# Kernel optimization log

Measured on AMD Instinct MI355X. Metric: run time of the kernel, lower is better.

## Reference

```python
import jax, jax.numpy as jnp
import numpy as np

N = 100_000   # nodes
D = 64        # hidden = H * C
H, C = 8, 8   # heads, per-head channels
E = 500_000   # edges per edge set
EPS = 1e-3    # keras LayerNormalization default epsilon
RSQRT_C = np.float32(1.0 / np.sqrt(C))


def setup_inputs() -> dict:
    key = jax.random.key(0)
    ks = jax.random.split(key, 13)
    s = 0.05
    return dict(
        x=jax.random.normal(ks[0], (N, D), jnp.float32),
        src0=jax.random.randint(ks[1], (E,), 0, N, jnp.int32),
        dst0=jax.random.randint(ks[2], (E,), 0, N, jnp.int32),
        src1=jax.random.randint(ks[3], (E,), 0, N, jnp.int32),
        dst1=jax.random.randint(ks[4], (E,), 0, N, jnp.int32),
        Wk=jax.random.normal(ks[5], (D, D), jnp.float32) * s,
        bk=jnp.zeros((D,), jnp.float32),
        Wm=jax.random.normal(ks[6], (D, D), jnp.float32) * s,
        bm=jnp.zeros((D,), jnp.float32),
        Wq=jax.random.normal(ks[7], (D, D), jnp.float32) * s,
        bq=jnp.zeros((D,), jnp.float32),
        Wa=jax.random.normal(ks[8], (D, D), jnp.float32) * s,
        ba=jnp.zeros((D,), jnp.float32),
        Watt0=jax.random.normal(ks[9], (H, C, C), jnp.float32) * s,
        Wmsg0=jax.random.normal(ks[10], (H, C, C), jnp.float32) * s,
        prior0=jnp.ones((H,), jnp.float32),
        Watt1=jax.random.normal(ks[11], (H, C, C), jnp.float32) * s,
        Wmsg1=jax.random.normal(ks[12], (H, C, C), jnp.float32) * s,
        prior1=jnp.ones((H,), jnp.float32),
        skip_w=jnp.ones((1,), jnp.float32),
        ln_gamma=jnp.ones((D,), jnp.float32),
        ln_beta=jnp.zeros((D,), jnp.float32),
    )


def _edge_terms(k, m, q, src, dst, Watt, Wmsg, prior):
    # gather sender keys/messages, apply per-edge-set per-head projections
    ke = jnp.einsum('ehk,hkl->ehl', k[src], Watt)          # [E,H,C]
    score = jnp.einsum('ehc,ehc->eh', ke, q[dst]) * prior * RSQRT_C  # [E,H]
    me = jnp.einsum('ehk,hkl->ehl', m[src], Wmsg)          # [E,H,C]
    return score, me


def _forward(x, src0, dst0, src1, dst1, Wk, bk, Wm, bm, Wq, bq, Wa, ba,
             Watt0, Wmsg0, prior0, Watt1, Wmsg1, prior1,
             skip_w, ln_gamma, ln_beta):
    n = x.shape[0]
    split = lambda t: t.reshape(n, H, C)
    k = split(x @ Wk + bk)   # sender keys   [N,H,C]
    m = split(x @ Wm + bm)   # sender msgs   [N,H,C]
    q = split(x @ Wq + bq)   # receiver qrys [N,H,C]

    s0, m0 = _edge_terms(k, m, q, src0, dst0, Watt0, Wmsg0, prior0)
    s1, m1 = _edge_terms(k, m, q, src1, dst1, Watt1, Wmsg1, prior1)

    # joint segment softmax over ALL incoming edges per receiver (across edge sets)
    scores = jnp.concatenate([s0, s1], axis=0)  # [Et,H]
    msgs = jnp.concatenate([m0, m1], axis=0)    # [Et,H,C]
    recv = jnp.concatenate([dst0, dst1], axis=0)
    smax = jax.ops.segment_max(scores, recv, num_segments=n)
    ex = jnp.exp(scores - smax[recv])
    denom = jax.ops.segment_sum(ex, recv, num_segments=n)
    coef = ex / denom[recv]                      # [Et,H]

    pooled = jax.ops.segment_sum(coef[:, :, None] * msgs, recv, num_segments=n)  # [N,H,C]
    merged = pooled.reshape(n, D)
    agg = jax.nn.gelu(merged, approximate=False) @ Wa + ba
    # (dropout_rate=0.0 -> identity)
    sc = jax.nn.sigmoid(skip_w[0])               # learnable weighted skip
    out = sc * agg + (1.0 - sc) * x
    # layer norm (keras default eps=1e-3)
    mu = jnp.mean(out, axis=-1, keepdims=True)
    var = jnp.var(out, axis=-1, keepdims=True)
    return ln_gamma * (out - mu) * jax.lax.rsqrt(var + EPS) + ln_beta


def reference(x, src0, dst0, src1, dst1, Wk, bk, Wm, bm, Wq, bq, Wa, ba,
              Watt0, Wmsg0, prior0, Watt1, Wmsg1, prior1,
              skip_w, ln_gamma, ln_beta):
    return _forward(x, src0, dst0, src1, dst1, Wk, bk, Wm, bm, Wq, bq, Wa, ba,
                    Watt0, Wmsg0, prior0, Watt1, Wmsg1, prior1,
                    skip_w, ln_gamma, ln_beta)
```

## Files before the change

kernel.cpp:

```cpp
#include <hip/hip_runtime.h>
#include <cstdint>
#include <cstddef>

#define TPB 256
static constexpr float RSQRT_C_F = 0.35355339059327373f;

typedef __attribute__((ext_vector_type(8))) short bf16x8;
typedef __attribute__((ext_vector_type(4))) float f32x4;

__device__ __forceinline__ unsigned short f2bf(float f) {
    unsigned u = __float_as_uint(f);
    u += 0x7FFFu + ((u >> 16) & 1u);
    return (unsigned short)(u >> 16);
}
__device__ __forceinline__ float bf2f(unsigned short h) {
    return __uint_as_float((unsigned)h << 16);
}
__device__ __forceinline__ float loF(unsigned u) { return __uint_as_float(u << 16); }
__device__ __forceinline__ float hiF(unsigned u) { return __uint_as_float(u); }

__global__ void prep1_kernel(const float* __restrict__ Wq, const float* __restrict__ bq,
                             const float* __restrict__ Wk, const float* __restrict__ bk,
                             const float* __restrict__ Wm, const float* __restrict__ bm,
                             const float* __restrict__ Watt0, const float* __restrict__ prior0,
                             const float* __restrict__ Watt1, const float* __restrict__ prior1,
                             const float* __restrict__ Wmsg0, const float* __restrict__ Wmsg1,
                             float* __restrict__ Wbig, float* __restrict__ bbig) {
    int idx = blockIdx.x * TPB + threadIdx.x;
    if (idx < 64 * 320) {
        int i = idx / 320, col = idx % 320;
        float v;
        if (col < 64) {
            v = Wq[i * 64 + col];
        } else {
            int j = col - 64, set = j >> 6, l = j & 63, h = l >> 3, lc = l & 7;
            const float* Win = (set < 2) ? Wk : Wm;
            const float* T = (set == 0) ? Watt0 : (set == 1) ? Watt1 : (set == 2) ? Wmsg0 : Wmsg1;
            float scale = (set == 0) ? prior0[h] * RSQRT_C_F
                        : (set == 1) ? prior1[h] * RSQRT_C_F : 1.f;
            float acc = 0.f;
            #pragma unroll
            for (int c = 0; c < 8; c++) acc += Win[i * 64 + h * 8 + c] * T[h * 64 + c * 8 + lc];
            v = acc * scale;
        }
        Wbig[idx] = v;
    } else if (idx < 64 * 320 + 320) {
        int col = idx - 64 * 320;
        float v;
        if (col < 64) {
            v = bq[col];
        } else {
            int j = col - 64, set = j >> 6, l = j & 63, h = l >> 3, lc = l & 7;
            const float* bin = (set < 2) ? bk : bm;
            const float* T = (set == 0) ? Watt0 : (set == 1) ? Watt1 : (set == 2) ? Wmsg0 : Wmsg1;
            float scale = (set == 0) ? prior0[h] * RSQRT_C_F
                        : (set == 1) ? prior1[h] * RSQRT_C_F : 1.f;
            float acc = 0.f;
            #pragma unroll
            for (int c = 0; c < 8; c++) acc += bin[h * 8 + c] * T[h * 64 + c * 8 + lc];
            v = acc * scale;
        }
        bbig[col] = v;
    }
}

__global__ void prep2_kernel(const float* __restrict__ Wbig, const float* __restrict__ Wa,
                             unsigned short* __restrict__ Wpack,
                             unsigned short* __restrict__ Wapack) {
    int p = blockIdx.x * TPB + threadIdx.x;
    bool isWa = (p >= 40 * 64);
    if (p >= 48 * 64) return;
    int pl = isWa ? p - 40 * 64 : p;
    int lane = pl & 63, ctkt = pl >> 6;
    int ct = ctkt >> 1, kt = ctkt & 1;
    int kbase = kt * 32 + (lane >> 4) * 8;
    int col = ct * 16 + (lane & 15);
    const float* W = isWa ? Wa : Wbig;
    const int stride = isWa ? 64 : 320;
    unsigned short h[8];
    #pragma unroll
    for (int j = 0; j < 8; j++) h[j] = f2bf(W[(size_t)(kbase + j) * stride + col]);
    uint4 pk;
    pk.x = (unsigned)h[0] | ((unsigned)h[1] << 16);
    pk.y = (unsigned)h[2] | ((unsigned)h[3] << 16);
    pk.z = (unsigned)h[4] | ((unsigned)h[5] << 16);
    pk.w = (unsigned)h[6] | ((unsigned)h[7] << 16);
    unsigned short* dst = isWa ? Wapack : Wpack;
    *(uint4*)&dst[(size_t)pl * 8] = pk;
}

__global__ void hist_kernel(const int* __restrict__ dst0, const int* __restrict__ dst1,
                            int* __restrict__ sub, int* __restrict__ rank,
                            int E0, int Etot, int N) {
    int e = blockIdx.x * TPB + threadIdx.x;
    if (e >= Etot) return;
    int d = (e < E0) ? dst0[e] : dst1[e - E0];
    d = min(max(d, 0), N - 1);
    int s = blockIdx.x & 7;
    rank[e] = atomicAdd(&sub[s * N + d], 1);
}

__global__ void sumsub_kernel(int* __restrict__ sub, int* __restrict__ count, int N) {
    int d = blockIdx.x * TPB + threadIdx.x;
    if (d >= N) return;
    int s = 0;
    #pragma unroll
    for (int b = 0; b < 8; b++) {
        int t = sub[b * N + d];
        sub[b * N + d] = s;
        s += t;
    }
    count[d] = s;
}

__global__ void scan1(const int* __restrict__ count, int* __restrict__ offsets,
                      int* __restrict__ blocksums, int n) {
    __shared__ int sums[TPB];
    int b = blockIdx.x, t = threadIdx.x;
    int base = b * 1024 + t * 4;
    int c0 = (base + 0 < n) ? count[base + 0] : 0;
    int c1 = (base + 1 < n) ? count[base + 1] : 0;
    int c2 = (base + 2 < n) ? count[base + 2] : 0;
    int c3 = (base + 3 < n) ? count[base + 3] : 0;
    int local = c0 + c1 + c2 + c3;
    sums[t] = local;
    __syncthreads();
    for (int off = 1; off < TPB; off <<= 1) {
        int add = (t >= off) ? sums[t - off] : 0;
        __syncthreads();
        sums[t] += add;
        __syncthreads();
    }
    int excl = sums[t] - local;
    if (base + 0 < n) offsets[base + 0] = excl;
    if (base + 1 < n) offsets[base + 1] = excl + c0;
    if (base + 2 < n) offsets[base + 2] = excl + c0 + c1;
    if (base + 3 < n) offsets[base + 3] = excl + c0 + c1 + c2;
    if (t == TPB - 1) blocksums[b] = sums[TPB - 1];
}

__global__ void scan2(int* __restrict__ blocksums, int nb) {
    __shared__ int s[TPB];
    int t = threadIdx.x;
    int v = (t < nb) ? blocksums[t] : 0;
    s[t] = v;
    __syncthreads();
    for (int off = 1; off < TPB; off <<= 1) {
        int add = (t >= off) ? s[t - off] : 0;
        __syncthreads();
        s[t] += add;
        __syncthreads();
    }
    if (t < nb) blocksums[t] = s[t] - v;
}

__global__ void scan3(int* __restrict__ offsets, const int* __restrict__ blocksums,
                      int* __restrict__ sub, int n, int Etot) {
    int i = blockIdx.x * TPB + threadIdx.x;
    if (i < n) {
        int v = offsets[i] + blocksums[i >> 10];
        offsets[i] = v;
        #pragma unroll
        for (int b = 0; b < 8; b++) sub[b * n + i] += v;
    }
    if (i == n) offsets[n] = Etot;
}

__global__ void scatter_kernel(const int* __restrict__ src0, const int* __restrict__ dst0,
                               const int* __restrict__ src1, const int* __restrict__ dst1,
                               const int* __restrict__ sub,
                               const int* __restrict__ rank, unsigned* __restrict__ records,
                               int E0, int Etot, int N) {
    int e = blockIdx.x * TPB + threadIdx.x;
    if (e >= Etot) return;
    int s, d, setbit;
    if (e < E0) { s = src0[e]; d = dst0[e]; setbit = 0; }
    else        { s = src1[e - E0]; d = dst1[e - E0]; setbit = 1; }
    d = min(max(d, 0), N - 1);
    int sb = (e >> 8) & 7;
    int pos = sub[sb * N + d] + rank[e];
    pos = min(max(pos, 0), Etot - 1);
    records[pos] = (unsigned)s | ((unsigned)setbit << 24);
}

__global__ __launch_bounds__(TPB) void proj_mfma(const float* __restrict__ x,
                                                 const unsigned short* __restrict__ Wpack,
                                                 const float* __restrict__ bbig,
                                                 unsigned short* __restrict__ qbuf,
                                                 unsigned short* __restrict__ kmbuf,
                                                 int N) {
    const int lane = threadIdx.x & 63;
    const int wv = threadIdx.x >> 6;
    const int rowbase = blockIdx.x * 64 + wv * 16;
    const int arow = min(rowbase + (lane & 15), N - 1);
    const int kbase = (lane >> 4) * 8;

    bf16x8 afrag[2];
    #pragma unroll
    for (int kt = 0; kt < 2; kt++) {
        const float* xp = x + (size_t)arow * 64 + kt * 32 + kbase;
        float4 v0 = *(const float4*)xp;
        float4 v1 = *(const float4*)(xp + 4);
        bf16x8 a;
        a[0] = (short)f2bf(v0.x); a[1] = (short)f2bf(v0.y);
        a[2] = (short)f2bf(v0.z); a[3] = (short)f2bf(v0.w);
        a[4] = (short)f2bf(v1.x); a[5] = (short)f2bf(v1.y);
        a[6] = (short)f2bf(v1.z); a[7] = (short)f2bf(v1.w);
        afrag[kt] = a;
    }

    const int colq = lane & 15;
    const int rgrp = (lane >> 4) * 4;

    for (int ct = 0; ct < 20; ct++) {
        bf16x8 b0 = *(const bf16x8*)(Wpack + ((size_t)(ct * 2 + 0) * 64 + lane) * 8);
        bf16x8 b1 = *(const bf16x8*)(Wpack + ((size_t)(ct * 2 + 1) * 64 + lane) * 8);
        f32x4 acc = {0.f, 0.f, 0.f, 0.f};
        acc = __builtin_amdgcn_mfma_f32_16x16x32_bf16(afrag[0], b0, acc, 0, 0, 0);
        acc = __builtin_amdgcn_mfma_f32_16x16x32_bf16(afrag[1], b1, acc, 0, 0, 0);
        const int col = ct * 16 + colq;
        const float bv = bbig[col];
        if (ct < 4) {
            #pragma unroll
            for (int r = 0; r < 4; r++) {
                int row = rowbase + rgrp + r;
                if (row < N) qbuf[(size_t)row * 64 + col] = f2bf(acc[r] + bv);
            }
        } else {
            const int kmcol = col - 64;
            #pragma unroll
            for (int r = 0; r < 4; r++) {
                int row = rowbase + rgrp + r;
                if (row < N) kmbuf[(size_t)row * 256 + kmcol] = f2bf(acc[r] + bv);
            }
        }
    }
}

__global__ __launch_bounds__(TPB) void pool_kernel(const unsigned short* __restrict__ qbuf,
                                                   const unsigned short* __restrict__ kmbuf,
                                                   const unsigned* __restrict__ records,
                                                   const int* __restrict__ offsets,
                                                   unsigned short* __restrict__ pooledN,
                                                   int N) {
    const int lane = threadIdx.x & 63;
    const int wid = (blockIdx.x * TPB + threadIdx.x) >> 6;
    if (wid >= N) return;
    const int beg = offsets[wid], end = offsets[wid + 1];

    const int e_idx = lane >> 3;
    const int j = lane & 7;

    uint4 qv = *(const uint4*)(qbuf + (size_t)wid * 64 + (j << 3));
    float qa0 = loF(qv.x), qa1 = hiF(qv.x), qa2 = loF(qv.y), qa3 = hiF(qv.y);
    float qa4 = loF(qv.z), qa5 = hiF(qv.z), qa6 = loF(qv.w), qa7 = hiF(qv.w);

    float d_run = 0.f;
    float p0 = 0.f, p1 = 0.f, p2 = 0.f, p3 = 0.f, p4 = 0.f, p5 = 0.f, p6 = 0.f, p7 = 0.f;

#define EDGE(T) {                                                              \
        unsigned rec = records[T];                                             \
        size_t base = ((size_t)(rec & 0xFFFFFFu) << 8) + (((rec >> 24) & 1u) << 6) + (j << 3); \
        uint4 kv = *(const uint4*)(kmbuf + base);                              \
        uint4 mv = *(const uint4*)(kmbuf + base + 128);                        \
        float s = loF(kv.x) * qa0 + hiF(kv.x) * qa1                            \
                + loF(kv.y) * qa2 + hiF(kv.y) * qa3                            \
                + loF(kv.z) * qa4 + hiF(kv.z) * qa5                            \
                + loF(kv.w) * qa6 + hiF(kv.w) * qa7;                           \
        float c = __expf(fminf(s, 60.f));                                      \
        d_run += c;                                                            \
        p0 += c * loF(mv.x); p1 += c * hiF(mv.x);                              \
        p2 += c * loF(mv.y); p3 += c * hiF(mv.y);                              \
        p4 += c * loF(mv.z); p5 += c * hiF(mv.z);                              \
        p6 += c * loF(mv.w); p7 += c * hiF(mv.w);                              \
    }

    int t = beg + e_idx;
    for (; t + 8 < end; t += 16) { EDGE(t); EDGE(t + 8); }
    if (t < end) EDGE(t);
#undef EDGE

    const bool loA = (e_idx & 4) == 0;
    float a0, a1, a2, a3;
    {
        float s0 = loA ? p4 : p0, s1 = loA ? p5 : p1;
        float s2 = loA ? p6 : p2, s3 = loA ? p7 : p3;
        a0 = (loA ? p0 : p4) + __shfl_xor(s0, 32, 64);
        a1 = (loA ? p1 : p5) + __shfl_xor(s1, 32, 64);
        a2 = (loA ? p2 : p6) + __shfl_xor(s2, 32, 64);
        a3 = (loA ? p3 : p7) + __shfl_xor(s3, 32, 64);
    }
    const bool loB = (e_idx & 2) == 0;
    float b0, b1;
    {
        float s0 = loB ? a2 : a0, s1 = loB ? a3 : a1;
        b0 = (loB ? a0 : a2) + __shfl_xor(s0, 16, 64);
        b1 = (loB ? a1 : a3) + __shfl_xor(s1, 16, 64);
    }
    const bool loC = (e_idx & 1) == 0;
    float r;
    {
        float s0 = loC ? b1 : b0;
        r = (loC ? b0 : b1) + __shfl_xor(s0, 8, 64);
    }
    d_run += __shfl_xor(d_run, 8, 64);
    d_run += __shfl_xor(d_run, 16, 64);
    d_run += __shfl_xor(d_run, 32, 64);

    const int ch = (j << 3) | e_idx;
    pooledN[(size_t)wid * 64 + ch] = f2bf((end > beg) ? r / d_run : 0.f);
}

__global__ __launch_bounds__(TPB) void final_mfma(const float* __restrict__ x,
                                                  const unsigned short* __restrict__ pooledN,
                                                  const unsigned short* __restrict__ Wapack,
                                                  const float* __restrict__ ba,
                                                  const float* __restrict__ skipw,
                                                  const float* __restrict__ gamma,
                                                  const float* __restrict__ beta,
                                                  float* __restrict__ out, int N) {
    const int lane = threadIdx.x & 63;
    const int wv = threadIdx.x >> 6;
    const int rowbase = blockIdx.x * 64 + wv * 16;
    const int arow = min(rowbase + (lane & 15), N - 1);
    const int kbase = (lane >> 4) * 8;
    const float sc = 1.f / (1.f + __expf(-skipw[0]));

    bf16x8 afrag[2];
    #pragma unroll
    for (int kt = 0; kt < 2; kt++) {
        uint4 pv = *(const uint4*)(pooledN + (size_t)arow * 64 + kt * 32 + kbase);
        float g[8];
        g[0] = loF(pv.x); g[1] = bf2f((unsigned short)(pv.x >> 16));
        g[2] = loF(pv.y); g[3] = bf2f((unsigned short)(pv.y >> 16));
        g[4] = loF(pv.z); g[5] = bf2f((unsigned short)(pv.z >> 16));
        g[6] = loF(pv.w); g[7] = bf2f((unsigned short)(pv.w >> 16));
        bf16x8 a;
        #pragma unroll
        for (int i = 0; i < 8; i++) {
            float gg = 0.5f * g[i] * (1.f + erff(g[i] * 0.70710678118654752f));
            a[i] = (short)f2bf(gg);
        }
        afrag[kt] = a;
    }

    const int colq = lane & 15;
    const int rgrp = (lane >> 4) * 4;

    float o[4][4];
    #pragma unroll
    for (int ct = 0; ct < 4; ct++) {
        bf16x8 b0 = *(const bf16x8*)(Wapack + ((size_t)(ct * 2 + 0) * 64 + lane) * 8);
        bf16x8 b1 = *(const bf16x8*)(Wapack + ((size_t)(ct * 2 + 1) * 64 + lane) * 8);
        f32x4 acc = {0.f, 0.f, 0.f, 0.f};
        acc = __builtin_amdgcn_mfma_f32_16x16x32_bf16(afrag[0], b0, acc, 0, 0, 0);
        acc = __builtin_amdgcn_mfma_f32_16x16x32_bf16(afrag[1], b1, acc, 0, 0, 0);
        const int col = ct * 16 + colq;
        const float bav = ba[col];
        #pragma unroll
        for (int r = 0; r < 4; r++) {
            int row = min(rowbase + rgrp + r, N - 1);
            float xv = x[(size_t)row * 64 + col];
            o[ct][r] = sc * (acc[r] + bav) + (1.f - sc) * xv;
        }
    }

    #pragma unroll
    for (int r = 0; r < 4; r++) {
        float s1 = o[0][r] + o[1][r] + o[2][r] + o[3][r];
        float s2 = o[0][r] * o[0][r] + o[1][r] * o[1][r]
                 + o[2][r] * o[2][r] + o[3][r] * o[3][r];
        #pragma unroll
        for (int off = 1; off <= 8; off <<= 1) {
            s1 += __shfl_xor(s1, off, 64);
            s2 += __shfl_xor(s2, off, 64);
        }
        float mu = s1 * (1.f / 64.f);
        float var = s2 * (1.f / 64.f) - mu * mu;
        float rs = rsqrtf(var + 1e-3f);
        const int row = rowbase + rgrp + r;
        if (row < N) {
            #pragma unroll
            for (int ct = 0; ct < 4; ct++) {
                const int col = ct * 16 + colq;
                out[(size_t)row * 64 + col] = gamma[col] * (o[ct][r] - mu) * rs + beta[col];
            }
        }
    }
}

extern "C" void kernel_launch(void* const* d_in, const int* in_sizes, int n_in,
                              void* d_out, int out_size, void* d_ws, size_t ws_size,
                              hipStream_t stream) {
    const float* x      = (const float*)d_in[0];
    const int*   src0   = (const int*)d_in[1];
    const int*   dst0   = (const int*)d_in[2];
    const int*   src1   = (const int*)d_in[3];
    const int*   dst1   = (const int*)d_in[4];
    const float* Wk     = (const float*)d_in[5];
    const float* bk     = (const float*)d_in[6];
    const float* Wm     = (const float*)d_in[7];
    const float* bm     = (const float*)d_in[8];
    const float* Wq     = (const float*)d_in[9];
    const float* bq     = (const float*)d_in[10];
    const float* Wa     = (const float*)d_in[11];
    const float* ba     = (const float*)d_in[12];
    const float* Watt0  = (const float*)d_in[13];
    const float* Wmsg0  = (const float*)d_in[14];
    const float* prior0 = (const float*)d_in[15];
    const float* Watt1  = (const float*)d_in[16];
    const float* Wmsg1  = (const float*)d_in[17];
    const float* prior1 = (const float*)d_in[18];
    const float* skipw  = (const float*)d_in[19];
    const float* gamma  = (const float*)d_in[20];
    const float* beta   = (const float*)d_in[21];

    const int N  = in_sizes[0] / 64;
    const int E0 = in_sizes[1];
    const int E1 = in_sizes[3];
    const int Etot = E0 + E1;

    float* ws       = (float*)d_ws;
    float* Wbig     = ws;
    float* bbig     = Wbig + 64 * 320;
    unsigned short* Wpack  = (unsigned short*)(bbig + 320);
    unsigned short* Wapack = Wpack + 40 * 64 * 8;
    unsigned short* qbuf   = Wapack + 8 * 64 * 8;
    unsigned short* pooledN = qbuf + (size_t)N * 64;
    unsigned short* kmbuf  = pooledN + (size_t)N * 64;
    int* sub        = (int*)(kmbuf + (size_t)N * 256);
    int* count      = sub + (size_t)8 * N;
    int* offsets    = count + N;
    int* blocksums  = offsets + N + 1;
    int* rank       = blocksums + 512;
    unsigned* records = (unsigned*)(rank + Etot);

    const int nb1 = (N + 1023) / 1024;
    const int gE = (Etot + TPB - 1) / TPB;

    prep1_kernel<<<(64 * 320 + 320 + TPB - 1) / TPB, TPB, 0, stream>>>(
        Wq, bq, Wk, bk, Wm, bm, Watt0, prior0, Watt1, prior1, Wmsg0, Wmsg1, Wbig, bbig);
    hipMemsetAsync(sub, 0, (size_t)8 * N * sizeof(int), stream);
    prep2_kernel<<<(48 * 64 + TPB - 1) / TPB, TPB, 0, stream>>>(Wbig, Wa, Wpack, Wapack);

    proj_mfma<<<(N + 63) / 64, TPB, 0, stream>>>(x, Wpack, bbig, qbuf, kmbuf, N);

    hist_kernel<<<gE, TPB, 0, stream>>>(dst0, dst1, sub, rank, E0, Etot, N);
    sumsub_kernel<<<(N + TPB - 1) / TPB, TPB, 0, stream>>>(sub, count, N);

    scan1<<<nb1, TPB, 0, stream>>>(count, offsets, blocksums, N);
    scan2<<<1, TPB, 0, stream>>>(blocksums, nb1);
    scan3<<<(N + 1 + TPB - 1) / TPB, TPB, 0, stream>>>(offsets, blocksums, sub, N, Etot);

    scatter_kernel<<<gE, TPB, 0, stream>>>(src0, dst0, src1, dst1, sub,
                                           rank, records, E0, Etot, N);

    pool_kernel<<<(N * 64 + TPB - 1) / TPB, TPB, 0, stream>>>(qbuf, kmbuf, records, offsets,
                                                              pooledN, N);

    final_mfma<<<(N + 63) / 64, TPB, 0, stream>>>(x, pooledN, Wapack, ba, skipw,
                                                  gamma, beta, (float*)d_out, N);
}
```

Before: 161.8 us.

## Assign one 8-lane group per node in pool kernel instead of a wavefront

The pooling kernel now maps each node to 8 lanes (one per head) rather than a full 64-lane wavefront, so each group walks its node's edges serially. This removes the cross-lane shuffle reduction and launches 8x fewer threads, and the output is written as one vectorized 16-byte store per lane. In exchange, parallelism per node drops, and lanes in a wavefront handle nodes with different in-degrees, so divergence and load imbalance rise. Gathers across different nodes in one wavefront may also coalesce less well.

Measured after the change: 163.0 us. No clear change (+0.7%).

```diff
diff --git a/kernel.cpp b/kernel.cpp
--- a/kernel.cpp
+++ b/kernel.cpp
@@ -244,14 +244,12 @@
                                                    unsigned short* __restrict__ pooledN,
                                                    int N) {
     const int lane = threadIdx.x & 63;
-    const int wid = (blockIdx.x * TPB + threadIdx.x) >> 6;
-    if (wid >= N) return;
-    const int beg = offsets[wid], end = offsets[wid + 1];
-
-    const int e_idx = lane >> 3;
     const int j = lane & 7;
-
-    uint4 qv = *(const uint4*)(qbuf + (size_t)wid * 64 + (j << 3));
+    const int r = ((blockIdx.x * TPB + threadIdx.x) >> 6) * 8 + (lane >> 3);
+    if (r >= N) return;
+    const int beg = offsets[r], end = offsets[r + 1];
+
+    uint4 qv = *(const uint4*)(qbuf + (size_t)r * 64 + (j << 3));
     float qa0 = loF(qv.x), qa1 = hiF(qv.x), qa2 = loF(qv.y), qa3 = hiF(qv.y);
     float qa4 = loF(qv.z), qa5 = hiF(qv.z), qa6 = loF(qv.w), qa7 = hiF(qv.w);
 
@@ -275,40 +273,18 @@
         p6 += c * loF(mv.w); p7 += c * hiF(mv.w);                              \
     }
 
-    int t = beg + e_idx;
-    for (; t + 8 < end; t += 16) { EDGE(t); EDGE(t + 8); }
+    int t = beg;
+    for (; t + 1 < end; t += 2) { EDGE(t); EDGE(t + 1); }
     if (t < end) EDGE(t);
 #undef EDGE
 
-    const bool loA = (e_idx & 4) == 0;
-    float a0, a1, a2, a3;
-    {
-        float s0 = loA ? p4 : p0, s1 = loA ? p5 : p1;
-        float s2 = loA ? p6 : p2, s3 = loA ? p7 : p3;
-        a0 = (loA ? p0 : p4) + __shfl_xor(s0, 32, 64);
-        a1 = (loA ? p1 : p5) + __shfl_xor(s1, 32, 64);
-        a2 = (loA ? p2 : p6) + __shfl_xor(s2, 32, 64);
-        a3 = (loA ? p3 : p7) + __shfl_xor(s3, 32, 64);
-    }
-    const bool loB = (e_idx & 2) == 0;
-    float b0, b1;
-    {
-        float s0 = loB ? a2 : a0, s1 = loB ? a3 : a1;
-        b0 = (loB ? a0 : a2) + __shfl_xor(s0, 16, 64);
-        b1 = (loB ? a1 : a3) + __shfl_xor(s1, 16, 64);
-    }
-    const bool loC = (e_idx & 1) == 0;
-    float r;
-    {
-        float s0 = loC ? b1 : b0;
-        r = (loC ? b0 : b1) + __shfl_xor(s0, 8, 64);
-    }
-    d_run += __shfl_xor(d_run, 8, 64);
-    d_run += __shfl_xor(d_run, 16, 64);
-    d_run += __shfl_xor(d_run, 32, 64);
-
-    const int ch = (j << 3) | e_idx;
-    pooledN[(size_t)wid * 64 + ch] = f2bf((end > beg) ? r / d_run : 0.f);
+    const float inv = (end > beg) ? 1.f / d_run : 0.f;
+    uint4 ov;
+    ov.x = (unsigned)f2bf(p0 * inv) | ((unsigned)f2bf(p1 * inv) << 16);
+    ov.y = (unsigned)f2bf(p2 * inv) | ((unsigned)f2bf(p3 * inv) << 16);
+    ov.z = (unsigned)f2bf(p4 * inv) | ((unsigned)f2bf(p5 * inv) << 16);
+    ov.w = (unsigned)f2bf(p6 * inv) | ((unsigned)f2bf(p7 * inv) << 16);
+    *(uint4*)(pooledN + (size_t)r * 64 + (j << 3)) = ov;
 }
 
 __global__ __launch_bounds__(TPB) void final_mfma(const float* __restrict__ x,
@@ -455,8 +431,8 @@
     scatter_kernel<<<gE, TPB, 0, stream>>>(src0, dst0, src1, dst1, sub,
                                            rank, records, E0, Etot, N);
 
-    pool_kernel<<<(N * 64 + TPB - 1) / TPB, TPB, 0, stream>>>(qbuf, kmbuf, records, offsets,
-                                                              pooledN, N);
+    pool_kernel<<<((size_t)N * 8 + TPB - 1) / TPB, TPB, 0, stream>>>(qbuf, kmbuf, records,
+                                                                     offsets, pooledN, N);
 
     final_mfma<<<(N + 63) / 64, TPB, 0, stream>>>(x, pooledN, Wapack, ba, skipw,
                                                   gamma, beta, (float*)d_out, N);
```
